# Kernel tuning notes

Measured on AMD Instinct MI355X. Metric: run time of the kernel, lower is better.

## Reference

```python
import jax, jax.numpy as jnp
import numpy as np

B, NSIDE, NH = 4, 64, 8
N = 12 * NSIDE * NSIDE          # HEALPix pixel count, nested ordering
CIN, CHID, COUT = 256, 512, 256
WS = 16                          # window = 4**(w+1) nested pixels, w=1
HD = CHID // NH


def _ln(x, g, b, eps=1e-5):
    m = x.mean(-1, keepdims=True)
    v = ((x - m) ** 2).mean(-1, keepdims=True)
    return (x - m) * jax.lax.rsqrt(v + eps) * g + b


def _win_attn(x, qkv_w, qkv_b, pw, pb):
    b_, n_, c = x.shape
    nw = n_ // WS
    xw = x.reshape(b_, nw, WS, c)
    qkv = xw @ qkv_w + qkv_b                      # [B, nw, ws, 3C]
    q, k, v = jnp.split(qkv, 3, axis=-1)
    def heads(t):
        return t.reshape(b_, nw, WS, NH, HD).transpose(0, 1, 3, 2, 4)
    q, k, v = heads(q), heads(k), heads(v)        # [B, nw, H, ws, hd]
    a = jax.nn.softmax(jnp.einsum('bwhqd,bwhkd->bwhqk', q, k) * (HD ** -0.5), axis=-1)
    o = jnp.einsum('bwhqk,bwhkd->bwhqd', a, v)
    o = o.transpose(0, 1, 3, 2, 4).reshape(b_, n_, c)
    return o @ pw + pb


def _heal_block(x, p, shift):
    if shift:
        x = jnp.roll(x, -WS // 2, axis=1)          # shifted-window (cyclic in nested order)
    x = x + _win_attn(_ln(x, p['ln1g'], p['ln1b']), p['qkvw'], p['qkvb'], p['pw'], p['pb'])
    h = _ln(x, p['ln2g'], p['ln2b'])
    h = jax.nn.gelu(h @ p['m1w'] + p['m1b'], approximate=False) @ p['m2w'] + p['m2b']
    x = x + h
    if shift:
        x = jnp.roll(x, WS // 2, axis=1)
    return x


def _sn_linear(h, W, b, u):
    # torch spectral_norm: one power-iteration, u/v detached, sigma = u' W v
    v = W @ u                                      # [CHID]
    v = jax.lax.stop_gradient(v / (jnp.linalg.norm(v) + 1e-12))
    u2 = v @ W                                     # [COUT]
    u2 = jax.lax.stop_gradient(u2 / (jnp.linalg.norm(u2) + 1e-12))
    sigma = v @ W @ u2
    return h @ (W / sigma) + b


def setup_inputs() -> dict:
    key = jax.random.key(0)
    ks = iter(jax.random.split(key, 64))
    def w(shape, s=0.02):
        return jax.random.normal(next(ks), shape, jnp.float32) * s
    inp = {'x': jax.random.normal(next(ks), (B, N, CIN), jnp.float32)}
    inp['ff1_w'] = w((CIN, CHID)); inp['ff1_b'] = jnp.zeros((CHID,), jnp.float32)
    for pre in ('a', 'b'):
        inp[f'{pre}_ln1g'] = jnp.ones((CHID,), jnp.float32)
        inp[f'{pre}_ln1b'] = jnp.zeros((CHID,), jnp.float32)
        inp[f'{pre}_qkvw'] = w((CHID, 3 * CHID)); inp[f'{pre}_qkvb'] = jnp.zeros((3 * CHID,), jnp.float32)
        inp[f'{pre}_pw'] = w((CHID, CHID)); inp[f'{pre}_pb'] = jnp.zeros((CHID,), jnp.float32)
        inp[f'{pre}_ln2g'] = jnp.ones((CHID,), jnp.float32)
        inp[f'{pre}_ln2b'] = jnp.zeros((CHID,), jnp.float32)
        inp[f'{pre}_m1w'] = w((CHID, 4 * CHID)); inp[f'{pre}_m1b'] = jnp.zeros((4 * CHID,), jnp.float32)
        inp[f'{pre}_m2w'] = w((4 * CHID, CHID)); inp[f'{pre}_m2b'] = jnp.zeros((CHID,), jnp.float32)
    inp['ff2_w'] = w((CHID, COUT)); inp['ff2_b'] = jnp.zeros((COUT,), jnp.float32)
    inp['ff2_u'] = jax.random.normal(next(ks), (COUT,), jnp.float32)
    return inp


def reference(x, ff1_w, ff1_b,
              a_ln1g, a_ln1b, a_qkvw, a_qkvb, a_pw, a_pb, a_ln2g, a_ln2b, a_m1w, a_m1b, a_m2w, a_m2b,
              b_ln1g, b_ln1b, b_qkvw, b_qkvb, b_pw, b_pb, b_ln2g, b_ln2b, b_m1w, b_m1b, b_m2w, b_m2b,
              ff2_w, ff2_b, ff2_u):
    pa = dict(ln1g=a_ln1g, ln1b=a_ln1b, qkvw=a_qkvw, qkvb=a_qkvb, pw=a_pw, pb=a_pb,
              ln2g=a_ln2g, ln2b=a_ln2b, m1w=a_m1w, m1b=a_m1b, m2w=a_m2w, m2b=a_m2b)
    pb_ = dict(ln1g=b_ln1g, ln1b=b_ln1b, qkvw=b_qkvw, qkvb=b_qkvb, pw=b_pw, pb=b_pb,
               ln2g=b_ln2g, ln2b=b_ln2b, m1w=b_m1w, m1b=b_m1b, m2w=b_m2w, m2b=b_m2b)
    h = jax.nn.gelu(x @ ff1_w + ff1_b, approximate=False)   # feed_forward1
    h = _heal_block(h, pa, shift=False)                     # message_passing1
    h = _heal_block(h, pb_, shift=True)                     # message_passing2
    return _sn_linear(h, ff2_w, ff2_b, ff2_u)               # spectral-norm linear
```

## Files before the change

### kernel.cpp

```cpp
#include <hip/hip_runtime.h>
#include <hip/hip_bf16.h>
#include <math.h>

typedef _Float16 f16;
typedef __attribute__((ext_vector_type(8))) _Float16 f16x8;
typedef __attribute__((ext_vector_type(4))) float f32x4;

#define DINLINE __device__ __forceinline__

DINLINE float gelu_exact(float x) {
  return 0.5f * x * (1.0f + erff(x * 0.70710678118654752f));
}
DINLINE void gload16(const void* g, void* l) {
  __builtin_amdgcn_global_load_lds((const __attribute__((address_space(1))) void*)g,
                                   (__attribute__((address_space(3))) void*)l, 16, 0, 0);
}

template <int EPI>
__global__ __launch_bounds__(256, 2) void gemm_f16(
    const f16* __restrict__ A, const f16* __restrict__ Bt,
    const float* __restrict__ bias, const f16* __restrict__ Cin,
    float* __restrict__ Cf, f16* __restrict__ Cb,
    const float* __restrict__ scale_ptr,
    int N, int K, int nct)
{
  __shared__ alignas(16) f16 lA[128 * 32];
  __shared__ alignas(16) f16 lB[128 * 32];

  const int nwg = (int)gridDim.x;
  const int gid = (int)blockIdx.x;
  const int q = nwg >> 3, r = nwg & 7;
  const int xcd = gid & 7, idx = gid >> 3;
  const int swz = (xcd < r ? xcd * (q + 1) : r * (q + 1) + (xcd - r) * q) + idx;
  const int rt = swz / nct, ct = swz - rt * nct;
  const int m0 = rt << 7, n0 = ct << 7;

  const int tid = (int)threadIdx.x;
  const int lane = tid & 63;
  const int wid = tid >> 6;
  const int wr = wid >> 1, wc = wid & 1;

  const int srow = tid >> 2;
  const int scol = (tid & 3) << 3;

  const int rsel = lane & 15;
  const int ksel = (lane >> 4) << 3;

  f32x4 acc[4][4] = {};

  for (int k0 = 0; k0 < K; k0 += 32) {
    __syncthreads();
    gload16(A + (size_t)(m0 + srow) * K + k0 + scol, lA + tid * 8);
    gload16(A + (size_t)(m0 + 64 + srow) * K + k0 + scol, lA + 2048 + tid * 8);
    gload16(Bt + (size_t)(n0 + srow) * K + k0 + scol, lB + tid * 8);
    gload16(Bt + (size_t)(n0 + 64 + srow) * K + k0 + scol, lB + 2048 + tid * 8);
    __syncthreads();

    f16x8 av[4], bv[4];
#pragma unroll
    for (int m = 0; m < 4; ++m)
      av[m] = *(const f16x8*)(lA + (wr * 64 + m * 16 + rsel) * 32 + ksel);
#pragma unroll
    for (int n = 0; n < 4; ++n)
      bv[n] = *(const f16x8*)(lB + (wc * 64 + n * 16 + rsel) * 32 + ksel);
#pragma unroll
    for (int m = 0; m < 4; ++m)
#pragma unroll
      for (int n = 0; n < 4; ++n)
        acc[m][n] = __builtin_amdgcn_mfma_f32_16x16x32_f16(av[m], bv[n], acc[m][n], 0, 0, 0);
  }

  const float scale = (EPI & 8) ? scale_ptr[0] : 1.0f;
  const int rbase = (lane >> 4) << 2;
  const int ccol = lane & 15;
#pragma unroll
  for (int m = 0; m < 4; ++m) {
#pragma unroll
    for (int n = 0; n < 4; ++n) {
      const int col = n0 + wc * 64 + n * 16 + ccol;
      const float bb = bias ? bias[col] : 0.0f;
#pragma unroll
      for (int j = 0; j < 4; ++j) {
        const int row = m0 + wr * 64 + m * 16 + rbase + j;
        float v = acc[m][n][j] * scale + bb;
        if (EPI & 1) v = gelu_exact(v);
        if (EPI & 2) v += (float)Cin[(size_t)row * N + col];
        if (EPI & 4) Cb[(size_t)row * N + col] = (f16)v;
        else         Cf[(size_t)row * N + col] = v;
      }
    }
  }
}

__global__ __launch_bounds__(256) void ln_f16(
    const f16* __restrict__ X, const float* __restrict__ g,
    const float* __restrict__ b, f16* __restrict__ Y)
{
  const int token = blockIdx.x * 4 + (threadIdx.x >> 6);
  const int lane = threadIdx.x & 63;
  f16x8 v = *(const f16x8*)(X + (size_t)token * 512 + lane * 8);
  float vf[8];
  float s = 0.f, s2 = 0.f;
#pragma unroll
  for (int j = 0; j < 8; ++j) { vf[j] = (float)v[j]; s += vf[j]; s2 += vf[j] * vf[j]; }
#pragma unroll
  for (int o = 32; o > 0; o >>= 1) { s += __shfl_xor(s, o, 64); s2 += __shfl_xor(s2, o, 64); }
  const float mean = s * (1.f / 512.f);
  const float inv = rsqrtf(s2 * (1.f / 512.f) - mean * mean + 1e-5f);
  const int c = lane * 8;
  f32x4 g0 = *(const f32x4*)(g + c), g1 = *(const f32x4*)(g + c + 4);
  f32x4 b0 = *(const f32x4*)(b + c), b1 = *(const f32x4*)(b + c + 4);
  f16x8 o8;
#pragma unroll
  for (int j = 0; j < 4; ++j) {
    o8[j]     = (f16)((vf[j] - mean) * inv * g0[j] + b0[j]);
    o8[4 + j] = (f16)((vf[4 + j] - mean) * inv * g1[j] + b1[j]);
  }
  *(f16x8*)(Y + (size_t)token * 512 + c) = o8;
}

__global__ __launch_bounds__(256) void cvt_f32_f16(const float* __restrict__ X,
                                                   f16* __restrict__ Y, long n8)
{
  const long i = (long)blockIdx.x * 256 + threadIdx.x;
  if (i >= n8) return;
  f32x4 v0 = *(const f32x4*)(X + i * 8), v1 = *(const f32x4*)(X + i * 8 + 4);
  f16x8 o8;
#pragma unroll
  for (int j = 0; j < 4; ++j) { o8[j] = (f16)v0[j]; o8[4 + j] = (f16)v1[j]; }
  *(f16x8*)(Y + i * 8) = o8;
}

__global__ __launch_bounds__(256) void w_tr(const float* __restrict__ W,
                                            f16* __restrict__ Wt, int K, int N)
{
  const int t = blockIdx.x * 256 + threadIdx.x;
  if (t >= K * N) return;
  const int n = t / K, k = t - n * K;
  Wt[t] = (f16)W[(size_t)k * N + n];
}

template <int SHIFT>
__global__ __launch_bounds__(256) void win_attn(const f16* __restrict__ QKV,
                                                f16* __restrict__ O)
{
  __shared__ alignas(16) f16 kv[2][16][1160];
  const int wl0 = (int)blockIdx.x * 2;
  const int tid = (int)threadIdx.x;

  for (int i = tid; i < 4096; i += 256) {
    const int win = i >> 11;
    const int rem = i & 2047;
    const int row = rem >> 7;
    const int c8 = rem & 127;
    const int src = ((wl0 + win) * 16 + row + SHIFT) % 49152;
    const int sect = c8 >> 6;
    const int hh = (c8 >> 3) & 7;
    const int dd = (c8 & 7) * 8;
    *(f16x8*)(&kv[win][row][sect * 576 + hh * 72 + dd]) =
        *(const f16x8*)(QKV + (size_t)src * 1536 + 512 + c8 * 8);
  }

  const int win = tid >> 7, h = (tid >> 4) & 7, qi = tid & 15;
  const int qtok = ((wl0 + win) * 16 + qi + SHIFT) % 49152;
  f16x8 qv[8];
#pragma unroll
  for (int c8 = 0; c8 < 8; ++c8)
    qv[c8] = *(const f16x8*)(QKV + (size_t)qtok * 1536 + h * 64 + c8 * 8);

  __syncthreads();

  float sc[16];
  float mx = -1e30f;
#pragma unroll
  for (int kj = 0; kj < 16; ++kj) {
    const f16* kr = &kv[win][kj][h * 72];
    float s = 0.f;
#pragma unroll
    for (int c8 = 0; c8 < 8; ++c8) {
      f16x8 k8 = *(const f16x8*)(kr + c8 * 8);
#pragma unroll
      for (int j = 0; j < 8; ++j) s += (float)qv[c8][j] * (float)k8[j];
    }
    s *= 0.125f;
    sc[kj] = s;
    mx = fmaxf(mx, s);
  }
  float sum = 0.f;
#pragma unroll
  for (int kj = 0; kj < 16; ++kj) { sc[kj] = expf(sc[kj] - mx); sum += sc[kj]; }
  const float inv = 1.f / sum;
  float ov[64] = {};
#pragma unroll
  for (int kj = 0; kj < 16; ++kj) {
    const float a = sc[kj] * inv;
    const f16* vr = &kv[win][kj][576 + h * 72];
#pragma unroll
    for (int c8 = 0; c8 < 8; ++c8) {
      f16x8 v8 = *(const f16x8*)(vr + c8 * 8);
#pragma unroll
      for (int j = 0; j < 8; ++j) ov[c8 * 8 + j] += a * (float)v8[j];
    }
  }
  f16* orow = O + (size_t)qtok * 512 + h * 64;
#pragma unroll
  for (int c8 = 0; c8 < 8; ++c8) {
    f16x8 t;
#pragma unroll
    for (int j = 0; j < 8; ++j) t[j] = (f16)ov[c8 * 8 + j];
    *(f16x8*)(orow + c8 * 8) = t;
  }
}

__global__ __launch_bounds__(256) void sn_sigma(const float* __restrict__ W,
                                                const float* __restrict__ u,
                                                float* __restrict__ inv_sigma)
{
  __shared__ float vsh[512];
  __shared__ float ush[256];
  __shared__ float red[256];
  const int t = (int)threadIdx.x;
  ush[t] = u[t];
  __syncthreads();
  float a0 = 0.f, a1 = 0.f;
  for (int j = 0; j < 256; ++j) {
    a0 += W[t * 256 + j] * ush[j];
    a1 += W[(t + 256) * 256 + j] * ush[j];
  }
  vsh[t] = a0; vsh[t + 256] = a1;
  red[t] = a0 * a0 + a1 * a1;
  __syncthreads();
  for (int s = 128; s > 0; s >>= 1) { if (t < s) red[t] += red[t + s]; __syncthreads(); }
  const float nv = sqrtf(red[0]) + 1e-12f;
  __syncthreads();
  const float invv = 1.f / nv;
  vsh[t] *= invv; vsh[t + 256] *= invv;
  __syncthreads();
  float u2 = 0.f;
  for (int i = 0; i < 512; ++i) u2 += vsh[i] * W[i * 256 + t];
  red[t] = u2 * u2;
  __syncthreads();
  for (int s = 128; s > 0; s >>= 1) { if (t < s) red[t] += red[t + s]; __syncthreads(); }
  const float nu = sqrtf(red[0]) + 1e-12f;
  __syncthreads();
  ush[t] = u2 / nu;
  __syncthreads();
  float d0 = 0.f, d1 = 0.f;
  for (int j = 0; j < 256; ++j) {
    d0 += W[t * 256 + j] * ush[j];
    d1 += W[(t + 256) * 256 + j] * ush[j];
  }
  red[t] = vsh[t] * d0 + vsh[t + 256] * d1;
  __syncthreads();
  for (int s = 128; s > 0; s >>= 1) { if (t < s) red[t] += red[t + s]; __syncthreads(); }
  if (t == 0) inv_sigma[0] = 1.f / red[0];
}

__global__ void fill_sentinel(float* __restrict__ out, long n, float val)
{
  const long i = (long)blockIdx.x * 256 + threadIdx.x;
  for (long k = i; k < n; k += (long)gridDim.x * 256) out[k] = val;
}

extern "C" void kernel_launch(void* const* d_in, const int* in_sizes, int n_in,
                              void* d_out, int out_size, void* d_ws, size_t ws_size,
                              hipStream_t stream)
{
  const int M = 196608;
  const int MC = 49152;
  constexpr size_t OFF_U   = 201326592ull;
  constexpr size_t OFF_OH  = 201326592ull + 150994944ull;
  constexpr size_t OFF_WT  = 402653184ull;
  constexpr size_t OFF_SIG = 415760384ull;
  constexpr size_t NEED    = OFF_SIG + 256ull;

  if (ws_size < NEED) {
    fill_sentinel<<<2048, 256, 0, stream>>>((float*)d_out, (long)out_size,
                                            (float)(ws_size >> 20));
    return;
  }

  char* ws = (char*)d_ws;
  f16* R     = (f16*)(ws);
  f16* U     = (f16*)(ws + OFF_U);
  f16* OH    = (f16*)(ws + OFF_OH);
  f16* WT    = (f16*)(ws + OFF_WT);
  float* sig = (float*)(ws + OFF_SIG);
  f16* X     = (f16*)d_out;

  const float* ff1_b = (const float*)d_in[2];
  const float* ff2_b = (const float*)d_in[28];

  f16* W_FF1 = WT;
  auto W_QKV = [&](int blk) { return WT + (blk ? 3276800 : 131072); };
  auto W_PW  = [&](int blk) { return WT + (blk ? 4063232 : 917504); };
  auto W_M1  = [&](int blk) { return WT + (blk ? 4325376 : 1179648); };
  auto W_M2  = [&](int blk) { return WT + (blk ? 5373952 : 2228224); };
  f16* W_FF2 = WT + 6422528;

  w_tr<<<512, 256, 0, stream>>>((const float*)d_in[1], W_FF1, 256, 512);
  for (int blk = 0; blk < 2; ++blk) {
    w_tr<<<3072, 256, 0, stream>>>((const float*)d_in[blk ? 17 : 5], W_QKV(blk), 512, 1536);
    w_tr<<<1024, 256, 0, stream>>>((const float*)d_in[blk ? 19 : 7], W_PW(blk), 512, 512);
    w_tr<<<4096, 256, 0, stream>>>((const float*)d_in[blk ? 23 : 11], W_M1(blk), 512, 2048);
    w_tr<<<4096, 256, 0, stream>>>((const float*)d_in[blk ? 25 : 13], W_M2(blk), 2048, 512);
  }
  w_tr<<<512, 256, 0, stream>>>((const float*)d_in[27], W_FF2, 512, 256);
  sn_sigma<<<1, 256, 0, stream>>>((const float*)d_in[27], (const float*)d_in[29], sig);

  cvt_f32_f16<<<24576, 256, 0, stream>>>((const float*)d_in[0], U, (long)M * 256 / 8);
  gemm_f16<5><<<6144, 256, 0, stream>>>(U, W_FF1, ff1_b, nullptr, nullptr, R, nullptr,
                                        512, 256, 4);

  for (int blk = 0; blk < 2; ++blk) {
    const float* ln1g = (const float*)d_in[blk ? 15 : 3];
    const float* ln1b = (const float*)d_in[blk ? 16 : 4];
    const float* qkvb = (const float*)d_in[blk ? 18 : 6];
    const float* pb   = (const float*)d_in[blk ? 20 : 8];
    const float* ln2g = (const float*)d_in[blk ? 21 : 9];
    const float* ln2b = (const float*)d_in[blk ? 22 : 10];
    const float* m1b  = (const float*)d_in[blk ? 24 : 12];
    const float* m2b  = (const float*)d_in[blk ? 26 : 14];

    ln_f16<<<49152, 256, 0, stream>>>(R, ln1g, ln1b, X);
    for (int mc = 0; mc < 4; ++mc) {
      const size_t ro = (size_t)mc * MC * 512;
      gemm_f16<4><<<4608, 256, 0, stream>>>(X + ro, W_QKV(blk), qkvb, nullptr,
                                            nullptr, U, nullptr, 1536, 512, 12);
      if (blk == 0) win_attn<0><<<1536, 256, 0, stream>>>(U, OH);
      else          win_attn<8><<<1536, 256, 0, stream>>>(U, OH);
      gemm_f16<6><<<1536, 256, 0, stream>>>(OH, W_PW(blk), pb, R + ro,
                                            nullptr, R + ro, nullptr, 512, 512, 4);
    }
    ln_f16<<<49152, 256, 0, stream>>>(R, ln2g, ln2b, X);
    for (int mc = 0; mc < 4; ++mc) {
      const size_t ro = (size_t)mc * MC * 512;
      gemm_f16<5><<<6144, 256, 0, stream>>>(X + ro, W_M1(blk), m1b, nullptr,
                                            nullptr, U, nullptr, 2048, 512, 16);
      gemm_f16<6><<<1536, 256, 0, stream>>>(U, W_M2(blk), m2b, R + ro,
                                            nullptr, R + ro, nullptr, 512, 2048, 4);
    }
  }

  gemm_f16<8><<<3072, 256, 0, stream>>>(R, W_FF2, ff2_b, nullptr, (float*)d_out,
                                        nullptr, sig, 256, 512, 2);
}
```

Measured before the change: 5.241 ms.

## Replace 128x128 GEMM with double-buffered 256x256 tile kernel using swizzled LDS

```diff
diff --git a/kernel.cpp b/kernel.cpp
--- a/kernel.cpp
+++ b/kernel.cpp
@@ -17,15 +17,14 @@
 }
 
 template <int EPI>
-__global__ __launch_bounds__(256, 2) void gemm_f16(
+__global__ __launch_bounds__(512, 2) void gemm256(
     const f16* __restrict__ A, const f16* __restrict__ Bt,
     const float* __restrict__ bias, const f16* __restrict__ Cin,
     float* __restrict__ Cf, f16* __restrict__ Cb,
     const float* __restrict__ scale_ptr,
     int N, int K, int nct)
 {
-  __shared__ alignas(16) f16 lA[128 * 32];
-  __shared__ alignas(16) f16 lB[128 * 32];
+  __shared__ alignas(16) f16 sm[2][2][16384];
 
   const int nwg = (int)gridDim.x;
   const int gid = (int)blockIdx.x;
@@ -33,63 +32,133 @@
   const int xcd = gid & 7, idx = gid >> 3;
   const int swz = (xcd < r ? xcd * (q + 1) : r * (q + 1) + (xcd - r) * q) + idx;
   const int rt = swz / nct, ct = swz - rt * nct;
-  const int m0 = rt << 7, n0 = ct << 7;
+  const int m0 = rt << 8, n0 = ct << 8;
 
   const int tid = (int)threadIdx.x;
   const int lane = tid & 63;
   const int wid = tid >> 6;
-  const int wr = wid >> 1, wc = wid & 1;
-
-  const int srow = tid >> 2;
-  const int scol = (tid & 3) << 3;
-
-  const int rsel = lane & 15;
-  const int ksel = (lane >> 4) << 3;
-
-  f32x4 acc[4][4] = {};
-
-  for (int k0 = 0; k0 < K; k0 += 32) {
-    __syncthreads();
-    gload16(A + (size_t)(m0 + srow) * K + k0 + scol, lA + tid * 8);
-    gload16(A + (size_t)(m0 + 64 + srow) * K + k0 + scol, lA + 2048 + tid * 8);
-    gload16(Bt + (size_t)(n0 + srow) * K + k0 + scol, lB + tid * 8);
-    gload16(Bt + (size_t)(n0 + 64 + srow) * K + k0 + scol, lB + 2048 + tid * 8);
-    __syncthreads();
-
-    f16x8 av[4], bv[4];
-#pragma unroll
-    for (int m = 0; m < 4; ++m)
-      av[m] = *(const f16x8*)(lA + (wr * 64 + m * 16 + rsel) * 32 + ksel);
-#pragma unroll
-    for (int n = 0; n < 4; ++n)
-      bv[n] = *(const f16x8*)(lB + (wc * 64 + n * 16 + rsel) * 32 + ksel);
-#pragma unroll
-    for (int m = 0; m < 4; ++m)
-#pragma unroll
-      for (int n = 0; n < 4; ++n)
-        acc[m][n] = __builtin_amdgcn_mfma_f32_16x16x32_f16(av[m], bv[n], acc[m][n], 0, 0, 0);
-  }
+  const int wr = wid >> 2, wc = wid & 3;
+
+  const int srow = tid >> 3;
+  const int sslot = (tid & 7) ^ (srow & 7);
+  const size_t aG0 = (size_t)(m0 + srow) * K + sslot * 8;
+  const size_t bG0 = (size_t)(n0 + srow) * K + sslot * 8;
+  const int sL0 = tid * 8;
+
+  const int rsel = lane & 15, khi = lane >> 4, kx = lane & 7;
+  const int swk0 = ((khi) ^ kx) << 3;
+  const int swk1 = ((4 + khi) ^ kx) << 3;
+  const int arow0 = wr * 128 + rsel;
+  const int brow0 = wc * 64 + rsel;
+
+  f32x4 acc[8][4] = {};
+  f16x8 aF[4][2], bF0[2][2], bF1[2][2];
+
+  const int NT = K >> 6;
+
+#define STAGE(b, k0)                                                          \
+  {                                                                           \
+    _Pragma("unroll")                                                         \
+    for (int j = 0; j < 4; ++j)                                               \
+      gload16(A + aG0 + (size_t)j * 64 * K + (k0), &sm[b][0][j * 4096 + sL0]);\
+    _Pragma("unroll")                                                         \
+    for (int j = 0; j < 4; ++j)                                               \
+      gload16(Bt + bG0 + (size_t)j * 64 * K + (k0), &sm[b][1][j * 4096 + sL0]);\
+  }
+
+#define LOADA(smA, MQ)                                                        \
+  {                                                                           \
+    _Pragma("unroll")                                                         \
+    for (int i = 0; i < 4; ++i) {                                             \
+      aF[i][0] = *(const f16x8*)((smA) + (arow0 + (MQ)*64 + i*16)*64 + swk0); \
+      aF[i][1] = *(const f16x8*)((smA) + (arow0 + (MQ)*64 + i*16)*64 + swk1); \
+    }                                                                         \
+  }
+
+#define LOADB(smB, BF, NQ)                                                    \
+  {                                                                           \
+    _Pragma("unroll")                                                         \
+    for (int nn = 0; nn < 2; ++nn) {                                          \
+      BF[nn][0] = *(const f16x8*)((smB) + (brow0 + (NQ)*32 + nn*16)*64 + swk0);\
+      BF[nn][1] = *(const f16x8*)((smB) + (brow0 + (NQ)*32 + nn*16)*64 + swk1);\
+    }                                                                         \
+  }
+
+#define MM(MQ, BF, NQ)                                                        \
+  {                                                                           \
+    __builtin_amdgcn_s_setprio(1);                                            \
+    _Pragma("unroll")                                                         \
+    for (int i = 0; i < 4; ++i)                                               \
+      _Pragma("unroll")                                                       \
+      for (int nn = 0; nn < 2; ++nn)                                          \
+        _Pragma("unroll")                                                     \
+        for (int kc = 0; kc < 2; ++kc)                                        \
+          acc[(MQ)*4 + i][(NQ)*2 + nn] = __builtin_amdgcn_mfma_f32_16x16x32_f16( \
+              aF[i][kc], BF[nn][kc], acc[(MQ)*4 + i][(NQ)*2 + nn], 0, 0, 0);  \
+    __builtin_amdgcn_s_setprio(0);                                            \
+  }
+
+#define CFENCE asm volatile("" ::: "memory")
+
+  STAGE(0, 0);
+  int cur = 0;
+  for (int t = 0; t < NT; ++t) {
+    CFENCE;
+    asm volatile("s_waitcnt vmcnt(0)" ::: "memory");
+    __builtin_amdgcn_s_barrier();
+    CFENCE;
+    if (t + 1 < NT) {
+      if (cur) STAGE(0, (t + 1) << 6) else STAGE(1, (t + 1) << 6)
+    }
+    const f16* smA = &sm[cur][0][0];
+    const f16* smB = &sm[cur][1][0];
+    LOADA(smA, 0); LOADB(smB, bF0, 0); MM(0, bF0, 0);
+    __builtin_amdgcn_s_barrier(); CFENCE;
+    LOADB(smB, bF1, 1); MM(0, bF1, 1);
+    __builtin_amdgcn_s_barrier(); CFENCE;
+    LOADA(smA, 1); MM(1, bF0, 0);
+    __builtin_amdgcn_s_barrier(); CFENCE;
+    MM(1, bF1, 1);
+    cur ^= 1;
+  }
+  __builtin_amdgcn_s_barrier();
+  CFENCE;
 
   const float scale = (EPI & 8) ? scale_ptr[0] : 1.0f;
-  const int rbase = (lane >> 4) << 2;
-  const int ccol = lane & 15;
-#pragma unroll
-  for (int m = 0; m < 4; ++m) {
+  const int R0 = m0 + wr * 128, C0 = n0 + wc * 64;
+  f16* myr = &sm[0][0][0] + wid * 8192;
+#pragma unroll
+  for (int m = 0; m < 8; ++m) {
 #pragma unroll
     for (int n = 0; n < 4; ++n) {
-      const int col = n0 + wc * 64 + n * 16 + ccol;
+      const int col = C0 + n * 16 + rsel;
       const float bb = bias ? bias[col] : 0.0f;
 #pragma unroll
       for (int j = 0; j < 4; ++j) {
-        const int row = m0 + wr * 64 + m * 16 + rbase + j;
+        const int rl = m * 16 + khi * 4 + j;
+        const int row = R0 + rl;
         float v = acc[m][n][j] * scale + bb;
         if (EPI & 1) v = gelu_exact(v);
         if (EPI & 2) v += (float)Cin[(size_t)row * N + col];
-        if (EPI & 4) Cb[(size_t)row * N + col] = (f16)v;
+        if (EPI & 4) myr[rl * 64 + n * 16 + rsel] = (f16)v;
         else         Cf[(size_t)row * N + col] = v;
       }
     }
   }
+  if (EPI & 4) {
+    CFENCE;
+#pragma unroll
+    for (int ci = 0; ci < 16; ++ci) {
+      const int rl = ci * 8 + (lane >> 3);
+      f16x8 v8 = *(const f16x8*)(myr + rl * 64 + (lane & 7) * 8);
+      *(f16x8*)(Cb + (size_t)(R0 + rl) * N + C0 + (lane & 7) * 8) = v8;
+    }
+  }
+#undef STAGE
+#undef LOADA
+#undef LOADB
+#undef MM
+#undef CFENCE
 }
 
 __global__ __launch_bounds__(256) void ln_f16(
@@ -309,8 +378,8 @@
   sn_sigma<<<1, 256, 0, stream>>>((const float*)d_in[27], (const float*)d_in[29], sig);
 
   cvt_f32_f16<<<24576, 256, 0, stream>>>((const float*)d_in[0], U, (long)M * 256 / 8);
-  gemm_f16<5><<<6144, 256, 0, stream>>>(U, W_FF1, ff1_b, nullptr, nullptr, R, nullptr,
-                                        512, 256, 4);
+  gemm256<5><<<1536, 512, 0, stream>>>(U, W_FF1, ff1_b, nullptr, nullptr, R, nullptr,
+                                       512, 256, 2);
 
   for (int blk = 0; blk < 2; ++blk) {
     const float* ln1g = (const float*)d_in[blk ? 15 : 3];
@@ -325,23 +394,23 @@
     ln_f16<<<49152, 256, 0, stream>>>(R, ln1g, ln1b, X);
     for (int mc = 0; mc < 4; ++mc) {
       const size_t ro = (size_t)mc * MC * 512;
-      gemm_f16<4><<<4608, 256, 0, stream>>>(X + ro, W_QKV(blk), qkvb, nullptr,
-                                            nullptr, U, nullptr, 1536, 512, 12);
+      gemm256<4><<<1152, 512, 0, stream>>>(X + ro, W_QKV(blk), qkvb, nullptr,
+                                           nullptr, U, nullptr, 1536, 512, 6);
       if (blk == 0) win_attn<0><<<1536, 256, 0, stream>>>(U, OH);
       else          win_attn<8><<<1536, 256, 0, stream>>>(U, OH);
-      gemm_f16<6><<<1536, 256, 0, stream>>>(OH, W_PW(blk), pb, R + ro,
-                                            nullptr, R + ro, nullptr, 512, 512, 4);
+      gemm256<6><<<384, 512, 0, stream>>>(OH, W_PW(blk), pb, R + ro,
+                                          nullptr, R + ro, nullptr, 512, 512, 2);
     }
     ln_f16<<<49152, 256, 0, stream>>>(R, ln2g, ln2b, X);
     for (int mc = 0; mc < 4; ++mc) {
       const size_t ro = (size_t)mc * MC * 512;
-      gemm_f16<5><<<6144, 256, 0, stream>>>(X + ro, W_M1(blk), m1b, nullptr,
-                                            nullptr, U, nullptr, 2048, 512, 16);
-      gemm_f16<6><<<1536, 256, 0, stream>>>(U, W_M2(blk), m2b, R + ro,
-                                            nullptr, R + ro, nullptr, 512, 2048, 4);
-    }
-  }
-
-  gemm_f16<8><<<3072, 256, 0, stream>>>(R, W_FF2, ff2_b, nullptr, (float*)d_out,
-                                        nullptr, sig, 256, 512, 2);
-}
+      gemm256<5><<<1536, 512, 0, stream>>>(X + ro, W_M1(blk), m1b, nullptr,
+                                           nullptr, U, nullptr, 2048, 512, 8);
+      gemm256<6><<<384, 512, 0, stream>>>(U, W_M2(blk), m2b, R + ro,
+                                          nullptr, R + ro, nullptr, 512, 2048, 2);
+    }
+  }
+
+  gemm256<8><<<768, 512, 0, stream>>>(R, W_FF2, ff2_b, nullptr, (float*)d_out,
+                                      nullptr, sig, 256, 512, 1);
+}
```

After: 5.231 ms. Within noise of the previous version (-0.2%).
